# Optimization experiments

Measured on AMD Instinct MI355X. Metric: run time of the kernel, lower is better.

Reference implementation:

```python
import jax, jax.numpy as jnp
import numpy as np

B, IN, H, OUT, RANK = 2048, 256, 128, 128, 8
EPS = 1e-5

def setup_inputs() -> dict:
    key = jax.random.key(0)
    ks = jax.random.split(key, 9)
    inv = lambda n: 1.0 / np.sqrt(n)
    return {
        "X": jax.random.normal(ks[0], (B, IN), jnp.float32),
        "W1": jax.random.uniform(ks[1], (IN, H), jnp.float32, -inv(IN), inv(IN)),
        "b1": jnp.zeros((H,), jnp.float32),
        "W2": jax.random.uniform(ks[2], (IN, OUT), jnp.float32, -inv(IN), inv(IN)),
        "b2": jnp.zeros((OUT,), jnp.float32),
        "W3": jax.random.uniform(ks[3], (H, OUT), jnp.float32, -inv(H), inv(H)),
        "b3": jnp.zeros((OUT,), jnp.float32),
        "P": jax.random.normal(ks[4], (RANK, H, H, H), jnp.float32),  # (rank, p, q, k)
        "gz": jnp.ones((H,), jnp.float32),
        "bz": jnp.zeros((H,), jnp.float32),
        "gy": jnp.ones((H,), jnp.float32),
        "by": jnp.zeros((H,), jnp.float32),
    }

def _bn(x, g, b):
    # training-mode BatchNorm1d: batch stats, biased variance
    m = x.mean(axis=0)
    v = x.var(axis=0)
    return (x - m) * jax.lax.rsqrt(v + EPS) * g + b

def reference(X, W1, b1, W2, b2, W3, b3, P, gz, bz, gy, by):
    Z = jax.nn.relu(X @ W1 + b1)               # (B, H); dropout = identity (eval)

    def step(carry, Pi):
        Zi, Y = carry
        # batch_quadratic: out[b,k] = sum_{p,q} Zi[b,p] * Pi[p,q,k] * Z[b,q]
        Zi = jnp.einsum('bp,pqk,bq->bk', Zi, Pi, Z)
        Zi = _bn(Zi, gz, bz)
        return (Zi, Y + Zi / RANK), None

    Y0 = jnp.zeros((X.shape[0], H), X.dtype)
    (_, Y), _ = jax.lax.scan(step, (Z, Y0), P)
    Y = _bn(Y, gy, by)
    out = jax.nn.relu(jax.nn.relu(Y @ W3 + b3) + jax.nn.relu(X @ W2 + b2))
    return out
```

## Files before the change

kernel.cpp:

```cpp
#include <hip/hip_runtime.h>

typedef __bf16 bf16x8 __attribute__((ext_vector_type(8)));
typedef float  floatx4 __attribute__((ext_vector_type(4)));

constexpr int B_    = 2048;
constexpr int NIN   = 256;
constexpr int H_    = 128;
constexpr int RANK_ = 8;
constexpr float EPS_ = 1e-5f;

__global__ __launch_bounds__(256)
void k_head(const float* __restrict__ X,
            const float* __restrict__ W1, const float* __restrict__ b1,
            const float* __restrict__ W2, const float* __restrict__ b2,
            const float* __restrict__ P,
            float* __restrict__ Z, float* __restrict__ R2, __bf16* __restrict__ Zbf,
            __bf16* __restrict__ Pperm, float* __restrict__ stats ) {
    __shared__ float sT[32 * 129];
    const int bx = blockIdx.x, t = threadIdx.x;

    if (bx < RANK_ + 1) stats[bx * 256 + t] = 0.f;

    {
        const int row0 = bx * 2;
        sT[t]       = X[(size_t)row0       * NIN + t];
        sT[256 + t] = X[(size_t)(row0 + 1) * NIN + t];
        __syncthreads();
        const int col = t & 127, half = t >> 7;
        float s1 = 0.f, s2 = 0.f;
        const float* sxh = sT + half * 256;
#pragma unroll 8
        for (int i = 0; i < NIN; ++i) {
            s1 = fmaf(sxh[i], W1[i * H_ + col], s1);
            s2 = fmaf(sxh[i], W2[i * H_ + col], s2);
        }
        const int b = row0 + half;
        const float z = fmaxf(s1 + b1[col], 0.f);
        const float r = fmaxf(s2 + b2[col], 0.f);
        Z[(size_t)b * H_ + col]   = z;
        Zbf[(size_t)b * H_ + col] = (__bf16)z;
        R2[(size_t)b * H_ + col]  = r;
        __syncthreads();
    }
    {
        const int r = bx >> 7, p = bx & 127;
        const float4* Pp4 = (const float4*)(P + ((size_t)r * H_ + p) * (H_ * H_));
        __bf16* dst = Pperm + (size_t)r * (H_ * H_ * H_);
        const int L = t & 63, quad = L >> 4, lo = L & 15, g0 = t >> 6;
#pragma unroll
        for (int s = 0; s < 4; ++s) {
#pragma unroll
            for (int it = 0; it < 4; ++it) {
                const int idx = it * 256 + t;
                const int q = idx >> 5, k4 = idx & 31;
                const float4 v = Pp4[(size_t)(s * 32 + q) * 32 + k4];
                float* d = sT + q * 129 + k4 * 4;
                d[0] = v.x; d[1] = v.y; d[2] = v.z; d[3] = v.w;
            }
            __syncthreads();
#pragma unroll
            for (int gg = 0; gg < 2; ++gg) {
                const int g = g0 + 4 * gg;
                __bf16 v8[8];
#pragma unroll
                for (int j = 0; j < 8; ++j)
                    v8[j] = (__bf16)sT[(quad * 8 + j) * 129 + g * 16 + lo];
                *(bf16x8*)(dst + (((size_t)(g * 128 + p) * 4 + s) * 64 + L) * 8) =
                    *(const bf16x8*)v8;
            }
            __syncthreads();
        }
    }
}

__global__ __launch_bounds__(512, 2)
void k_rank(const __bf16* __restrict__ Pr, const __bf16* __restrict__ Zbf,
            const float* __restrict__ prevT, const float* __restrict__ prevStats,
            const float* __restrict__ gz, const float* __restrict__ bz,
            float* __restrict__ T, float* __restrict__ stats, const int first) {
    __shared__ float smem[8960];
    const int kg = blockIdx.x, mblk = blockIdx.y, b0 = mblk * 64;
    const int t = threadIdx.x;
    const int w = t >> 6, L = t & 63, quad = L >> 4, lo = L & 15;

    float* sAl = smem + 8704; float* sBe = smem + 8832;
    if (t < 128) {
        if (first) { sAl[t] = 1.f; sBe[t] = 0.f; }
        else {
            const float s1 = prevStats[t], s2 = prevStats[128 + t];
            const float mm = s1 * (1.f / B_);
            const float var = s2 * (1.f / B_) - mm * mm;
            const float a = rsqrtf(var + EPS_) * gz[t];
            sAl[t] = a; sBe[t] = bz[t] - mm * a;
        }
    }
    bf16x8 A[4][4];
#pragma unroll
    for (int mt = 0; mt < 4; ++mt)
#pragma unroll
        for (int ks = 0; ks < 4; ++ks)
            A[mt][ks] = *(const bf16x8*)(Zbf + (size_t)(b0 + mt * 16 + lo) * H_ + ks * 32 + quad * 8);
    __syncthreads();
    {
        const int sp = t & 127, rr = t >> 7;
        const float a = sAl[sp], be = sBe[sp];
#pragma unroll
        for (int i = 0; i < 16; ++i) {
            const int row = rr + 4 * i;
            smem[sp * 68 + row] = fmaf(prevT[(size_t)(b0 + row) * H_ + sp], a, be);
        }
    }
    __syncthreads();

    floatx4 acc[4];
#pragma unroll
    for (int mt = 0; mt < 4; ++mt) acc[mt] = (floatx4){0.f, 0.f, 0.f, 0.f};

    const bf16x8* Pb = (const bf16x8*)Pr;
    const int p0 = w * 16;
    const size_t fbase = ((size_t)kg * 128 + p0) * 4;
    bf16x8 Bf[4], Bn[4];
#pragma unroll
    for (int s = 0; s < 4; ++s) Bf[s] = Pb[(fbase + s) * 64 + L];

    for (int pp = 0; pp < 16; ++pp) {
        const int p = p0 + pp;
        if (pp < 15) {
#pragma unroll
            for (int s = 0; s < 4; ++s)
                Bn[s] = Pb[(fbase + (size_t)(pp + 1) * 4 + s) * 64 + L];
        }
        floatx4 S[4];
#pragma unroll
        for (int mt = 0; mt < 4; ++mt) S[mt] = (floatx4){0.f, 0.f, 0.f, 0.f};
#pragma unroll
        for (int ks = 0; ks < 4; ++ks)
#pragma unroll
            for (int mt = 0; mt < 4; ++mt)
                S[mt] = __builtin_amdgcn_mfma_f32_16x16x32_bf16(A[mt][ks], Bf[ks], S[mt], 0, 0, 0);
#pragma unroll
        for (int mt = 0; mt < 4; ++mt) {
            const floatx4 zi = *(const floatx4*)&smem[p * 68 + mt * 16 + quad * 4];
            acc[mt] += zi * S[mt];
        }
#pragma unroll
        for (int s = 0; s < 4; ++s) Bf[s] = Bn[s];
    }
    __syncthreads();
#pragma unroll
    for (int mt = 0; mt < 4; ++mt)
#pragma unroll
        for (int i = 0; i < 4; ++i)
            smem[w * 1024 + (mt * 4 + i) * 64 + L] = acc[mt][i];
    if (t < 32) smem[8192 + t] = 0.f;
    __syncthreads();

    float cs = 0.f, cs2 = 0.f;
#pragma unroll
    for (int k2 = 0; k2 < 2; ++k2) {
        const int e = t + 512 * k2;
        float v = 0.f;
#pragma unroll
        for (int q = 0; q < 8; ++q) v += smem[q * 1024 + e];
        const int j = e >> 6, L2 = e & 63;
        const int row = b0 + (j >> 2) * 16 + (L2 >> 4) * 4 + (j & 3);
        const int col = kg * 16 + (L2 & 15);
        T[(size_t)row * H_ + col] = v;
        cs += v; cs2 += v * v;
    }
    cs  += __shfl_xor(cs, 16);  cs  += __shfl_xor(cs, 32);
    cs2 += __shfl_xor(cs2, 16); cs2 += __shfl_xor(cs2, 32);
    if (L < 16) { atomicAdd(&smem[8192 + L], cs); atomicAdd(&smem[8208 + L], cs2); }
    __syncthreads();
    if (t < 16)      atomicAdd(&stats[kg * 16 + t],            smem[8192 + t]);
    else if (t < 32) atomicAdd(&stats[128 + kg * 16 + t - 16], smem[8192 + t]);
}

__global__ __launch_bounds__(256)
void k_y(const float* __restrict__ T, const float* __restrict__ sums,
         const float* __restrict__ gz, const float* __restrict__ bz,
         float* __restrict__ Y, float* __restrict__ ysums) {
    __shared__ float al[1024], be[1024], red[256];
    const int bx = blockIdx.x, t = threadIdx.x;
    for (int e = t; e < 1024; e += 256) {
        const int rr = e >> 7, k = e & 127;
        const float s1 = sums[rr * 256 + k], s2 = sums[rr * 256 + 128 + k];
        const float mm = s1 * (1.f / B_);
        const float var = s2 * (1.f / B_) - mm * mm;
        const float a = rsqrtf(var + EPS_) * gz[k];
        al[e] = a; be[e] = bz[k] - mm * a;
    }
    red[t] = 0.f;
    __syncthreads();
    const int col = t & 127, half = t >> 7;
    float ps = 0.f, ps2 = 0.f;
    for (int i = 0; i < 16; ++i) {
        const int b = bx * 32 + half + 2 * i;
        float y = 0.f;
#pragma unroll
        for (int rr = 0; rr < 8; ++rr)
            y += fmaf(T[(size_t)rr * B_ * H_ + (size_t)b * H_ + col],
                      al[rr * 128 + col], be[rr * 128 + col]);
        y *= (1.f / RANK_);
        Y[(size_t)b * H_ + col] = y;
        ps += y; ps2 += y * y;
    }
    atomicAdd(&red[col],       half == 0 ? ps  : 0.f);
    atomicAdd(&red[128 + col], half == 0 ? ps2 : 0.f);
    __syncthreads();
    atomicAdd(&red[col],       half == 1 ? ps  : 0.f);
    atomicAdd(&red[128 + col], half == 1 ? ps2 : 0.f);
    __syncthreads();
    if (t < 128) {
        atomicAdd(&ysums[t],       red[t]);
        atomicAdd(&ysums[128 + t], red[128 + t]);
    }
}

__global__ __launch_bounds__(256)
void k_out(const float* __restrict__ Y, const float* __restrict__ ystats,
           const float* __restrict__ gy, const float* __restrict__ by,
           const float* __restrict__ W3, const float* __restrict__ b3,
           const float* __restrict__ R2, float* __restrict__ out) {
    __shared__ float sy[8 * 132];
    const int bx = blockIdx.x, t = threadIdx.x;
    const int col = t & 127, rh = t >> 7;
    const int b0 = bx * 8;
    const float mm = ystats[col] * (1.f / B_);
    const float var = ystats[128 + col] * (1.f / B_) - mm * mm;
    const float ay = rsqrtf(var + EPS_) * gy[col];
    const float bb = by[col] - mm * ay;
#pragma unroll
    for (int i = 0; i < 4; ++i) {
        const int row = rh + 2 * i;
        sy[row * 132 + col] = fmaf(Y[(size_t)(b0 + row) * H_ + col], ay, bb);
    }
    __syncthreads();
#pragma unroll
    for (int j = 0; j < 4; ++j) {
        const int row = rh * 4 + j;
        float s = 0.f;
        const float* syr = sy + row * 132;
#pragma unroll 8
        for (int h = 0; h < H_; ++h)
            s = fmaf(syr[h], W3[h * H_ + col], s);
        const size_t gi = (size_t)(b0 + row) * H_ + col;
        out[gi] = fmaxf(fmaxf(s + b3[col], 0.f) + R2[gi], 0.f);
    }
}

extern "C" void kernel_launch(void* const* d_in, const int* in_sizes, int n_in,
                              void* d_out, int out_size, void* d_ws, size_t ws_size,
                              hipStream_t stream) {
    const float* X  = (const float*)d_in[0];
    const float* W1 = (const float*)d_in[1];
    const float* b1 = (const float*)d_in[2];
    const float* W2 = (const float*)d_in[3];
    const float* b2 = (const float*)d_in[4];
    const float* W3 = (const float*)d_in[5];
    const float* b3 = (const float*)d_in[6];
    const float* P  = (const float*)d_in[7];
    const float* gz = (const float*)d_in[8];
    const float* bz = (const float*)d_in[9];
    const float* gy = (const float*)d_in[10];
    const float* by = (const float*)d_in[11];
    float* out = (float*)d_out;

    const size_t rankElems = (size_t)H_ * H_ * H_;

    char* wsb = (char*)d_ws;
    float* Z      = (float*)wsb;   wsb += (size_t)B_ * H_ * 4;
    float* R2     = (float*)wsb;   wsb += (size_t)B_ * H_ * 4;
    float* Y      = (float*)wsb;   wsb += (size_t)B_ * H_ * 4;
    float* stats  = (float*)wsb;   wsb += (size_t)(RANK_ + 1) * 256 * 4;
    float* T      = (float*)wsb;   wsb += (size_t)RANK_ * B_ * H_ * 4;
    __bf16* Zbf   = (__bf16*)wsb;  wsb += (size_t)B_ * H_ * 2;
    __bf16* Pperm = (__bf16*)wsb;

    float* ysums = stats + RANK_ * 256;

    k_head<<<1024, 256, 0, stream>>>(X, W1, b1, W2, b2, P, Z, R2, Zbf, Pperm, stats);

    for (int r = 0; r < RANK_; ++r) {
        const float* prevT = (r == 0) ? Z : (T + (size_t)(r - 1) * B_ * H_);
        const float* prevS = (r == 0) ? stats : (stats + (r - 1) * 256);
        k_rank<<<dim3(8, 32), 512, 0, stream>>>(Pperm + (size_t)r * rankElems, Zbf,
                                                prevT, prevS, gz, bz,
                                                T + (size_t)r * B_ * H_, stats + r * 256,
                                                r == 0 ? 1 : 0);
    }

    k_y<<<64, 256, 0, stream>>>(T, stats, gz, bz, Y, ysums);
    k_out<<<256, 256, 0, stream>>>(Y, ysums, gy, by, W3, b3, R2, out);
}
```

Baseline: 303.1 us.

## Retile head GEMM, widen rank blocks to 1024 threads, accumulate Y incrementally

The head kernel now computes X·W1 and X·W2 in only one block of every four, with 8 rows per block and W tiles staged through shared memory, so weights are reused across rows instead of reloaded from global memory per pair of rows. The rank kernel moves to 1024 threads with 16 waves, each handling 8 p-slices without the register double-buffer, and reduces 16 partials per output. Y is built up inside the rank kernels as each normalized previous-rank output is read, so the final Y kernel only handles the last rank. The trade-offs are lower occupancy and less load prefetching in the rank kernel, and extra Y read-modify-write traffic from the kg==0 blocks.

```diff
diff --git a/kernel.cpp b/kernel.cpp
--- a/kernel.cpp
+++ b/kernel.cpp
@@ -16,33 +16,59 @@
             const float* __restrict__ P,
             float* __restrict__ Z, float* __restrict__ R2, __bf16* __restrict__ Zbf,
             __bf16* __restrict__ Pperm, float* __restrict__ stats ) {
-    __shared__ float sT[32 * 129];
+    __shared__ float smem[10240];
     const int bx = blockIdx.x, t = threadIdx.x;
 
     if (bx < RANK_ + 1) stats[bx * 256 + t] = 0.f;
 
+    if ((bx & 3) == 0) {
+        const int b0 = (bx >> 2) * 8;
+        float* sX  = smem;
+        float* sW1 = smem + 2048;
+        float* sW2 = smem + 6144;
+        for (int e = t; e < 2048; e += 256) {
+            const int row = e >> 8, i = e & 255;
+            sX[e] = X[(size_t)(b0 + row) * NIN + i];
+        }
+        const int col = t & 127, rh = t >> 7;
+        float s1[4] = {0.f, 0.f, 0.f, 0.f}, s2[4] = {0.f, 0.f, 0.f, 0.f};
+        for (int c = 0; c < 8; ++c) {
+            __syncthreads();
+#pragma unroll
+            for (int q = 0; q < 4; ++q) {
+                const int idx = q * 256 + t;
+                const int i = idx >> 5, c4 = idx & 31;
+                *(float4*)&sW1[i * 128 + c4 * 4] =
+                    *(const float4*)&W1[(size_t)(c * 32 + i) * H_ + c4 * 4];
+                *(float4*)&sW2[i * 128 + c4 * 4] =
+                    *(const float4*)&W2[(size_t)(c * 32 + i) * H_ + c4 * 4];
+            }
+            __syncthreads();
+#pragma unroll 4
+            for (int i = 0; i < 32; ++i) {
+                const float w1 = sW1[i * 128 + col];
+                const float w2 = sW2[i * 128 + col];
+#pragma unroll
+                for (int j = 0; j < 4; ++j) {
+                    const float x = sX[(rh * 4 + j) * 256 + c * 32 + i];
+                    s1[j] = fmaf(x, w1, s1[j]);
+                    s2[j] = fmaf(x, w2, s2[j]);
+                }
+            }
+        }
+#pragma unroll
+        for (int j = 0; j < 4; ++j) {
+            const int b = b0 + rh * 4 + j;
+            const float z = fmaxf(s1[j] + b1[col], 0.f);
+            const float r = fmaxf(s2[j] + b2[col], 0.f);
+            Z[(size_t)b * H_ + col]   = z;
+            Zbf[(size_t)b * H_ + col] = (__bf16)z;
+            R2[(size_t)b * H_ + col]  = r;
+        }
+        __syncthreads();
+    }
     {
-        const int row0 = bx * 2;
-        sT[t]       = X[(size_t)row0       * NIN + t];
-        sT[256 + t] = X[(size_t)(row0 + 1) * NIN + t];
-        __syncthreads();
-        const int col = t & 127, half = t >> 7;
-        float s1 = 0.f, s2 = 0.f;
-        const float* sxh = sT + half * 256;
-#pragma unroll 8
-        for (int i = 0; i < NIN; ++i) {
-            s1 = fmaf(sxh[i], W1[i * H_ + col], s1);
-            s2 = fmaf(sxh[i], W2[i * H_ + col], s2);
-        }
-        const int b = row0 + half;
-        const float z = fmaxf(s1 + b1[col], 0.f);
-        const float r = fmaxf(s2 + b2[col], 0.f);
-        Z[(size_t)b * H_ + col]   = z;
-        Zbf[(size_t)b * H_ + col] = (__bf16)z;
-        R2[(size_t)b * H_ + col]  = r;
-        __syncthreads();
-    }
-    {
+        float* sT = smem;
         const int r = bx >> 7, p = bx & 127;
         const float4* Pp4 = (const float4*)(P + ((size_t)r * H_ + p) * (H_ * H_));
         __bf16* dst = Pperm + (size_t)r * (H_ * H_ * H_);
@@ -73,19 +99,20 @@
     }
 }
 
-__global__ __launch_bounds__(512, 2)
+__global__ __launch_bounds__(1024, 1)
 void k_rank(const __bf16* __restrict__ Pr, const __bf16* __restrict__ Zbf,
             const float* __restrict__ prevT, const float* __restrict__ prevStats,
             const float* __restrict__ gz, const float* __restrict__ bz,
-            float* __restrict__ T, float* __restrict__ stats, const int first) {
-    __shared__ float smem[8960];
+            float* __restrict__ T, float* __restrict__ stats,
+            float* __restrict__ Y, const int ymode) {
+    __shared__ float smem[16672];
     const int kg = blockIdx.x, mblk = blockIdx.y, b0 = mblk * 64;
     const int t = threadIdx.x;
     const int w = t >> 6, L = t & 63, quad = L >> 4, lo = L & 15;
 
-    float* sAl = smem + 8704; float* sBe = smem + 8832;
+    float* sAl = smem + 16384; float* sBe = smem + 16512;
     if (t < 128) {
-        if (first) { sAl[t] = 1.f; sBe[t] = 0.f; }
+        if (ymode == 0) { sAl[t] = 1.f; sBe[t] = 0.f; }
         else {
             const float s1 = prevStats[t], s2 = prevStats[128 + t];
             const float mm = s1 * (1.f / B_);
@@ -105,9 +132,14 @@
         const int sp = t & 127, rr = t >> 7;
         const float a = sAl[sp], be = sBe[sp];
 #pragma unroll
-        for (int i = 0; i < 16; ++i) {
-            const int row = rr + 4 * i;
-            smem[sp * 68 + row] = fmaf(prevT[(size_t)(b0 + row) * H_ + sp], a, be);
+        for (int i = 0; i < 8; ++i) {
+            const int row = rr + 8 * i;
+            const float zin = fmaf(prevT[(size_t)(b0 + row) * H_ + sp], a, be);
+            smem[sp * 68 + row] = zin;
+            if (kg == 0 && ymode != 0) {
+                float* yp = Y + (size_t)(b0 + row) * H_ + sp;
+                *yp = (ymode == 1) ? zin * (1.f / RANK_) : fmaf(zin, 1.f / RANK_, *yp);
+            }
         }
     }
     __syncthreads();
@@ -117,34 +149,22 @@
     for (int mt = 0; mt < 4; ++mt) acc[mt] = (floatx4){0.f, 0.f, 0.f, 0.f};
 
     const bf16x8* Pb = (const bf16x8*)Pr;
-    const int p0 = w * 16;
-    const size_t fbase = ((size_t)kg * 128 + p0) * 4;
-    bf16x8 Bf[4], Bn[4];
-#pragma unroll
-    for (int s = 0; s < 4; ++s) Bf[s] = Pb[(fbase + s) * 64 + L];
-
-    for (int pp = 0; pp < 16; ++pp) {
-        const int p = p0 + pp;
-        if (pp < 15) {
-#pragma unroll
-            for (int s = 0; s < 4; ++s)
-                Bn[s] = Pb[(fbase + (size_t)(pp + 1) * 4 + s) * 64 + L];
-        }
-        floatx4 S[4];
-#pragma unroll
-        for (int mt = 0; mt < 4; ++mt) S[mt] = (floatx4){0.f, 0.f, 0.f, 0.f};
-#pragma unroll
-        for (int ks = 0; ks < 4; ++ks)
-#pragma unroll
-            for (int mt = 0; mt < 4; ++mt)
-                S[mt] = __builtin_amdgcn_mfma_f32_16x16x32_bf16(A[mt][ks], Bf[ks], S[mt], 0, 0, 0);
+    const size_t wb = ((size_t)kg * 128 + w * 8) * 4;
+    for (int pp = 0; pp < 8; ++pp) {
+        bf16x8 Bf[4];
+#pragma unroll
+        for (int s = 0; s < 4; ++s)
+            Bf[s] = Pb[(wb + (size_t)pp * 4 + s) * 64 + L];
+        const int p = w * 8 + pp;
 #pragma unroll
         for (int mt = 0; mt < 4; ++mt) {
+            floatx4 S = (floatx4){0.f, 0.f, 0.f, 0.f};
+#pragma unroll
+            for (int ks = 0; ks < 4; ++ks)
+                S = __builtin_amdgcn_mfma_f32_16x16x32_bf16(A[mt][ks], Bf[ks], S, 0, 0, 0);
             const floatx4 zi = *(const floatx4*)&smem[p * 68 + mt * 16 + quad * 4];
-            acc[mt] += zi * S[mt];
-        }
-#pragma unroll
-        for (int s = 0; s < 4; ++s) Bf[s] = Bn[s];
+            acc[mt] += zi * S;
+        }
     }
     __syncthreads();
 #pragma unroll
@@ -152,57 +172,48 @@
 #pragma unroll
         for (int i = 0; i < 4; ++i)
             smem[w * 1024 + (mt * 4 + i) * 64 + L] = acc[mt][i];
-    if (t < 32) smem[8192 + t] = 0.f;
-    __syncthreads();
-
-    float cs = 0.f, cs2 = 0.f;
-#pragma unroll
-    for (int k2 = 0; k2 < 2; ++k2) {
-        const int e = t + 512 * k2;
-        float v = 0.f;
-#pragma unroll
-        for (int q = 0; q < 8; ++q) v += smem[q * 1024 + e];
-        const int j = e >> 6, L2 = e & 63;
-        const int row = b0 + (j >> 2) * 16 + (L2 >> 4) * 4 + (j & 3);
-        const int col = kg * 16 + (L2 & 15);
-        T[(size_t)row * H_ + col] = v;
-        cs += v; cs2 += v * v;
-    }
+    if (t < 32) smem[16640 + t] = 0.f;
+    __syncthreads();
+
+    float v = 0.f;
+#pragma unroll
+    for (int q = 0; q < 16; ++q) v += smem[q * 1024 + t];
+    const int j = t >> 6, L2 = t & 63;
+    const int row = b0 + (j >> 2) * 16 + (L2 >> 4) * 4 + (j & 3);
+    const int col = kg * 16 + (L2 & 15);
+    T[(size_t)row * H_ + col] = v;
+    float cs = v, cs2 = v * v;
     cs  += __shfl_xor(cs, 16);  cs  += __shfl_xor(cs, 32);
     cs2 += __shfl_xor(cs2, 16); cs2 += __shfl_xor(cs2, 32);
-    if (L < 16) { atomicAdd(&smem[8192 + L], cs); atomicAdd(&smem[8208 + L], cs2); }
-    __syncthreads();
-    if (t < 16)      atomicAdd(&stats[kg * 16 + t],            smem[8192 + t]);
-    else if (t < 32) atomicAdd(&stats[128 + kg * 16 + t - 16], smem[8192 + t]);
+    if (L2 < 16) { atomicAdd(&smem[16640 + L2], cs); atomicAdd(&smem[16656 + L2], cs2); }
+    __syncthreads();
+    if (t < 16)      atomicAdd(&stats[kg * 16 + t],            smem[16640 + t]);
+    else if (t < 32) atomicAdd(&stats[128 + kg * 16 + t - 16], smem[16640 + t]);
 }
 
 __global__ __launch_bounds__(256)
-void k_y(const float* __restrict__ T, const float* __restrict__ sums,
+void k_y(const float* __restrict__ T7, const float* __restrict__ s7,
          const float* __restrict__ gz, const float* __restrict__ bz,
          float* __restrict__ Y, float* __restrict__ ysums) {
-    __shared__ float al[1024], be[1024], red[256];
+    __shared__ float sAl[128], sBe[128], red[256];
     const int bx = blockIdx.x, t = threadIdx.x;
-    for (int e = t; e < 1024; e += 256) {
-        const int rr = e >> 7, k = e & 127;
-        const float s1 = sums[rr * 256 + k], s2 = sums[rr * 256 + 128 + k];
+    if (t < 128) {
+        const float s1 = s7[t], s2 = s7[128 + t];
         const float mm = s1 * (1.f / B_);
         const float var = s2 * (1.f / B_) - mm * mm;
-        const float a = rsqrtf(var + EPS_) * gz[k];
-        al[e] = a; be[e] = bz[k] - mm * a;
+        const float a = rsqrtf(var + EPS_) * gz[t];
+        sAl[t] = a; sBe[t] = bz[t] - mm * a;
     }
     red[t] = 0.f;
     __syncthreads();
     const int col = t & 127, half = t >> 7;
+    const float a = sAl[col], be = sBe[col];
     float ps = 0.f, ps2 = 0.f;
     for (int i = 0; i < 16; ++i) {
         const int b = bx * 32 + half + 2 * i;
-        float y = 0.f;
-#pragma unroll
-        for (int rr = 0; rr < 8; ++rr)
-            y += fmaf(T[(size_t)rr * B_ * H_ + (size_t)b * H_ + col],
-                      al[rr * 128 + col], be[rr * 128 + col]);
-        y *= (1.f / RANK_);
-        Y[(size_t)b * H_ + col] = y;
+        const size_t gi = (size_t)b * H_ + col;
+        const float y = Y[gi] + fmaf(T7[gi], a, be) * (1.f / RANK_);
+        Y[gi] = y;
         ps += y; ps2 += y * y;
     }
     atomicAdd(&red[col],       half == 0 ? ps  : 0.f);
@@ -284,12 +295,13 @@
     for (int r = 0; r < RANK_; ++r) {
         const float* prevT = (r == 0) ? Z : (T + (size_t)(r - 1) * B_ * H_);
         const float* prevS = (r == 0) ? stats : (stats + (r - 1) * 256);
-        k_rank<<<dim3(8, 32), 512, 0, stream>>>(Pperm + (size_t)r * rankElems, Zbf,
-                                                prevT, prevS, gz, bz,
-                                                T + (size_t)r * B_ * H_, stats + r * 256,
-                                                r == 0 ? 1 : 0);
-    }
-
-    k_y<<<64, 256, 0, stream>>>(T, stats, gz, bz, Y, ysums);
+        const int ymode = (r == 0) ? 0 : (r == 1 ? 1 : 2);
+        k_rank<<<dim3(8, 32), 1024, 0, stream>>>(Pperm + (size_t)r * rankElems, Zbf,
+                                                 prevT, prevS, gz, bz,
+                                                 T + (size_t)r * B_ * H_, stats + r * 256,
+                                                 Y, ymode);
+    }
+
+    k_y<<<64, 256, 0, stream>>>(T + (size_t)7 * B_ * H_, stats + 7 * 256, gz, bz, Y, ysums);
     k_out<<<256, 256, 0, stream>>>(Y, ysums, gy, by, W3, b3, R2, out);
 }
```

Result: slower. 324.2 us (+6.9%).
